# Performance work log

Measured on AMD Instinct MI355X. Metric: run time of the kernel, lower is better.

## Reference

```python
import jax, jax.numpy as jnp
import numpy as np


def setup_inputs() -> dict:
    key = jax.random.key(0)
    ks = jax.random.split(key, 8)
    n_videos, emb_dim = 200000, 128
    n_nodes, k_neigh = 20000, 32
    sc = 1.0 / np.sqrt(emb_dim)
    return {
        "video_embeddings": jax.random.normal(ks[0], (n_videos, emb_dim), jnp.float32),
        "video_nodes": jax.random.randint(ks[1], (n_nodes,), 0, n_videos, jnp.int64 if jax.config.jax_enable_x64 else jnp.int32),
        "neigh_idx": jax.random.randint(ks[2], (n_nodes, k_neigh), 0, n_videos, jnp.int64 if jax.config.jax_enable_x64 else jnp.int32),
        "W1": jax.random.normal(ks[3], (2 * emb_dim, emb_dim), jnp.float32) * sc,
        "b1": jnp.zeros((emb_dim,), jnp.float32),
        "W2": jax.random.normal(ks[4], (emb_dim, emb_dim), jnp.float32) * sc,
        "b2": jnp.zeros((emb_dim,), jnp.float32),
        "W3": jax.random.normal(ks[5], (emb_dim, 1), jnp.float32) * sc,
        "b3": jnp.zeros((1,), jnp.float32),
    }


def reference(video_embeddings, video_nodes, neigh_idx, W1, b1, W2, b2, W3, b3):
    # Ragged per-node loop vectorized as a padded [N, K] neighbor gather.
    neigh_emb = video_embeddings[neigh_idx]          # [N, K, D]
    node_emb = video_embeddings[video_nodes]         # [N, D]
    n, k, d = neigh_emb.shape
    # Attention MLP: cat(neigh, node_repeated) -> relu -> relu -> scalar score
    x = jnp.concatenate([neigh_emb, jnp.broadcast_to(node_emb[:, None, :], (n, k, d))], axis=-1)  # [N, K, 2D]
    h = jax.nn.relu(jnp.einsum("nke,ed->nkd", x, W1) + b1)
    h = jax.nn.relu(jnp.einsum("nke,ed->nkd", h, W2) + b2)
    scores = (jnp.einsum("nkd,do->nko", h, W3) + b3)[..., 0]  # [N, K]
    att = jax.nn.softmax(scores, axis=-1)                      # softmax over neighbors
    # Weighted aggregation: embed_matrix[i] = neigh_emb[i].T @ att[i]
    return jnp.einsum("nkd,nk->nd", neigh_emb, att)
```

## Files before the change

kernel.cpp:

```cpp
#include <hip/hip_runtime.h>
#include <hip/hip_bf16.h>

#define D  128
#define KN 32

typedef __attribute__((ext_vector_type(8))) short bf16x8;
typedef __attribute__((ext_vector_type(4))) float f32x4;

static __device__ __forceinline__ unsigned short f2bf(float f) {
    union { float f; unsigned int u; } v; v.f = f;
    unsigned int u = v.u;
    u += 0x7fff + ((u >> 16) & 1);
    return (unsigned short)(u >> 16);
}
static __device__ __forceinline__ float bf2f(unsigned short h) {
    union { float f; unsigned int u; } v; v.u = ((unsigned int)h) << 16;
    return v.f;
}

__global__ __launch_bounds__(256) void wt_kernel(
    const float* __restrict__ W1, const float* __restrict__ W2,
    unsigned short* __restrict__ W1Tt, unsigned short* __restrict__ W1Tb,
    unsigned short* __restrict__ W2T)
{
    int idx = blockIdx.x * 256 + threadIdx.x;
    if (idx < D * D) {
        int col = idx >> 7, e = idx & 127;
        W1Tt[col * D + e] = f2bf(W1[e * D + col]);
        W1Tb[col * D + e] = f2bf(W1[(D + e) * D + col]);
        W2T [col * D + e] = f2bf(W2[e * D + col]);
    }
}

__global__ __launch_bounds__(256) void p1q_kernel(
    const float* __restrict__ emb, const int* __restrict__ vnodes,
    int NV, int NN, int nvBlocks,
    const unsigned short* __restrict__ W1Tt, const unsigned short* __restrict__ W1Tb,
    const float* __restrict__ b1,
    unsigned short* __restrict__ P1, unsigned short* __restrict__ Q,
    unsigned short* __restrict__ EB)
{
    __shared__ unsigned short sA[128][136];

    const int tid  = threadIdx.x;
    const int lane = tid & 63;
    const int w    = tid >> 6;
    const int m    = lane & 15, q = lane >> 4;

    const bool nv = (int)blockIdx.x < nvBlocks;
    const int  bi = nv ? blockIdx.x : blockIdx.x - nvBlocks;
    const int  M  = nv ? NV : NN;
    const unsigned short* WT = nv ? W1Tt : W1Tb;
    const int r0 = bi * 128;

    int maxRows = M - r0; if (maxRows > 128) maxRows = 128;
    const int maxB = maxRows << 8;

#pragma unroll
    for (int i = 0; i < 16; ++i) {
        int e = tid + 256 * i;
        int row = e >> 5, c4 = (e & 31) << 2;
        int r = r0 + row; if (r > M - 1) r = M - 1;
        int vr = nv ? r : vnodes[r];
        const float4 f = *(const float4*)(emb + (long)vr * D + c4);
        ushort4 h;
        h.x = f2bf(f.x); h.y = f2bf(f.y); h.z = f2bf(f.z); h.w = f2bf(f.w);
        *(ushort4*)(&sA[row][c4]) = h;
    }
    __syncthreads();

    if (nv) {
        char* ebBase = (char*)(EB + (long)r0 * D);
#pragma unroll
        for (int j = 0; j < 8; ++j) {
            int p = j * 4096 + tid * 16;
            if (p < maxB) {
                int row = p >> 8, off = (p & 255) >> 1;
                *(bf16x8*)(ebBase + p) = *(const bf16x8*)(&sA[row][off]);
            }
        }
    }

    bf16x8 Bf[2][4];
#pragma unroll
    for (int nt = 0; nt < 2; ++nt)
#pragma unroll
        for (int kk = 0; kk < 4; ++kk)
            Bf[nt][kk] = *(const bf16x8*)(WT + (32 * w + 16 * nt + m) * D + kk * 32 + q * 8);
    float bv[2];
#pragma unroll
    for (int nt = 0; nt < 2; ++nt) bv[nt] = nv ? 0.f : b1[32 * w + 16 * nt + m];

    f32x4 acc[8][2];
#pragma unroll
    for (int mt = 0; mt < 8; ++mt)
#pragma unroll
        for (int nt = 0; nt < 2; ++nt) acc[mt][nt] = (f32x4){0.f, 0.f, 0.f, 0.f};

#pragma unroll
    for (int kk = 0; kk < 4; ++kk) {
#pragma unroll
        for (int mt = 0; mt < 8; ++mt) {
            bf16x8 a = *(const bf16x8*)(&sA[16 * mt + m][kk * 32 + q * 8]);
            acc[mt][0] = __builtin_amdgcn_mfma_f32_16x16x32_bf16(a, Bf[0][kk], acc[mt][0], 0, 0, 0);
            acc[mt][1] = __builtin_amdgcn_mfma_f32_16x16x32_bf16(a, Bf[1][kk], acc[mt][1], 0, 0, 0);
        }
    }

    __syncthreads();
#pragma unroll
    for (int mt = 0; mt < 8; ++mt)
#pragma unroll
        for (int nt = 0; nt < 2; ++nt) {
            int col = 32 * w + 16 * nt + m;
#pragma unroll
            for (int r = 0; r < 4; ++r)
                sA[16 * mt + 4 * q + r][col] = f2bf(acc[mt][nt][r] + bv[nt]);
        }
    __syncthreads();
    {
        char* dstBase = (char*)((nv ? P1 : Q) + (long)r0 * D);
#pragma unroll
        for (int j = 0; j < 8; ++j) {
            int p = j * 4096 + tid * 16;
            if (p < maxB) {
                int row = p >> 8, off = (p & 255) >> 1;
                *(bf16x8*)(dstBase + p) = *(const bf16x8*)(&sA[row][off]);
            }
        }
    }
}

__global__ __launch_bounds__(256, 3) void agg_kernel(
    const unsigned short* __restrict__ EB, const int* __restrict__ nidx,
    const unsigned short* __restrict__ W2T, const float* __restrict__ b2,
    const float* __restrict__ W3, const float* __restrict__ b3,
    const unsigned short* __restrict__ P1, const unsigned short* __restrict__ Q,
    float* __restrict__ out, int NN)
{
    __shared__ unsigned short sX[128][136];
    __shared__ float sSp[4][128];
    __shared__ float sAtt[128];

    const int tid  = threadIdx.x;
    const int lane = tid & 63;
    const int w    = tid >> 6;
    const int m    = lane & 15, q = lane >> 4;
    const int g4   = q;
    const int c    = m;

    bf16x8 Bf[2][4];
#pragma unroll
    for (int nt = 0; nt < 2; ++nt)
#pragma unroll
        for (int kk = 0; kk < 4; ++kk)
            Bf[nt][kk] = *(const bf16x8*)(W2T + (32 * w + 16 * nt + m) * D + kk * 32 + q * 8);
    float b2v[2], w3v[2];
#pragma unroll
    for (int nt = 0; nt < 2; ++nt) {
        int col = 32 * w + 16 * nt + m;
        b2v[nt] = b2[col];
        w3v[nt] = W3[col];
    }
    const float b3s = b3[0];

    const int groups = (NN + 3) >> 2;

    int g = blockIdx.x;
    int ni[8];
    bf16x8 pf[8];
    if (g < groups) {
        int nd = g * 4 + w; if (nd > NN - 1) nd = NN - 1;
#pragma unroll
        for (int j = 0; j < 8; ++j) {
            ni[j] = nidx[nd * KN + 4 * j + g4];
            pf[j] = *(const bf16x8*)(P1 + (long)ni[j] * D + c * 8);
        }
    }

    for (; g < groups; g += gridDim.x) {
        const int node0 = g * 4;
        int nd = node0 + w; if (nd > NN - 1) nd = NN - 1;

        {
            const bf16x8 qv = *(const bf16x8*)(Q + (long)nd * D + c * 8);
#pragma unroll
            for (int j = 0; j < 8; ++j) {
                bf16x8 r;
#pragma unroll
                for (int h = 0; h < 8; ++h) {
                    float v = bf2f((unsigned short)pf[j][h]) + bf2f((unsigned short)qv[h]);
                    r[h] = (short)f2bf(v > 0.f ? v : 0.f);
                }
                *(bf16x8*)(&sX[w * 32 + 4 * j + g4][c * 8]) = r;
            }
        }

        const int gn = g + gridDim.x;
        const bool more = gn < groups;
        int nin[8];
        if (more) {
            int ndn = gn * 4 + w; if (ndn > NN - 1) ndn = NN - 1;
#pragma unroll
            for (int j = 0; j < 8; ++j) nin[j] = nidx[ndn * KN + 4 * j + g4];
        }

        if (more) {
#pragma unroll
            for (int j = 0; j < 8; ++j)
                pf[j] = *(const bf16x8*)(P1 + (long)nin[j] * D + c * 8);
        }
        __syncthreads();

#pragma unroll
        for (int hv = 0; hv < 2; ++hv) {
            f32x4 acc[4][2];
#pragma unroll
            for (int mt = 0; mt < 4; ++mt) {
                acc[mt][0] = (f32x4){0.f, 0.f, 0.f, 0.f};
                acc[mt][1] = (f32x4){0.f, 0.f, 0.f, 0.f};
            }
#pragma unroll
            for (int kk = 0; kk < 4; ++kk) {
#pragma unroll
                for (int mt = 0; mt < 4; ++mt) {
                    bf16x8 a = *(const bf16x8*)(&sX[16 * (4 * hv + mt) + m][kk * 32 + q * 8]);
                    acc[mt][0] = __builtin_amdgcn_mfma_f32_16x16x32_bf16(a, Bf[0][kk], acc[mt][0], 0, 0, 0);
                    acc[mt][1] = __builtin_amdgcn_mfma_f32_16x16x32_bf16(a, Bf[1][kk], acc[mt][1], 0, 0, 0);
                }
            }
#pragma unroll
            for (int mt = 0; mt < 4; ++mt) {
                float p[4];
#pragma unroll
                for (int r = 0; r < 4; ++r) {
                    float h0 = acc[mt][0][r] + b2v[0]; h0 = h0 > 0.f ? h0 : 0.f;
                    float h1 = acc[mt][1][r] + b2v[1]; h1 = h1 > 0.f ? h1 : 0.f;
                    p[r] = h0 * w3v[0] + h1 * w3v[1];
                }
#pragma unroll
                for (int off = 8; off >= 1; off >>= 1)
#pragma unroll
                    for (int r = 0; r < 4; ++r) p[r] += __shfl_xor(p[r], off, 16);
                if (m == 0) {
#pragma unroll
                    for (int r = 0; r < 4; ++r) sSp[w][16 * (4 * hv + mt) + 4 * q + r] = p[r];
                }
            }
        }

        bf16x8 gv[8];
#pragma unroll
        for (int j = 0; j < 8; ++j)
            gv[j] = *(const bf16x8*)(EB + (long)ni[j] * D + c * 8);
        __syncthreads();

        if (tid < 128) {
            float s = sSp[0][tid] + sSp[1][tid] + sSp[2][tid] + sSp[3][tid] + b3s;
            float mx = s;
#pragma unroll
            for (int off = 16; off >= 1; off >>= 1) mx = fmaxf(mx, __shfl_xor(mx, off, 32));
            float e = __expf(s - mx);
            float sum = e;
#pragma unroll
            for (int off = 16; off >= 1; off >>= 1) sum += __shfl_xor(sum, off, 32);
            sAtt[tid] = e / sum;
        }
        __syncthreads();

        {
            float r8[8] = {0.f, 0.f, 0.f, 0.f, 0.f, 0.f, 0.f, 0.f};
#pragma unroll
            for (int j = 0; j < 8; ++j) {
                float a = sAtt[w * KN + 4 * j + g4];
#pragma unroll
                for (int h = 0; h < 8; ++h)
                    r8[h] += a * bf2f((unsigned short)gv[j][h]);
            }
#pragma unroll
            for (int h = 0; h < 8; ++h) {
                r8[h] += __shfl_xor(r8[h], 16);
                r8[h] += __shfl_xor(r8[h], 32);
            }
            int ndw = node0 + w;
            if (g4 == 0 && ndw < NN) {
                float4 o0 = {r8[0], r8[1], r8[2], r8[3]};
                float4 o1 = {r8[4], r8[5], r8[6], r8[7]};
                *(float4*)(out + (long)ndw * D + c * 8)     = o0;
                *(float4*)(out + (long)ndw * D + c * 8 + 4) = o1;
            }
        }
#pragma unroll
        for (int j = 0; j < 8; ++j) ni[j] = nin[j];
    }
}

__global__ __launch_bounds__(128) void naive_kernel(
    const float* __restrict__ emb, const int* __restrict__ vnodes,
    const int* __restrict__ nidx,
    const float* __restrict__ W1, const float* __restrict__ b1,
    const float* __restrict__ W2, const float* __restrict__ b2,
    const float* __restrict__ W3, const float* __restrict__ b3,
    float* __restrict__ out)
{
    __shared__ float sE[KN + 1][D];
    __shared__ float sH[KN][D];
    __shared__ float sH2[KN][D];
    __shared__ float sS[KN];
    __shared__ float sA2[KN];
    const int node = blockIdx.x, tid = threadIdx.x;

    for (int r = 0; r < KN + 1; ++r) {
        int vr = (r < KN) ? nidx[node * KN + r] : vnodes[node];
        sE[r][tid] = emb[(long)vr * D + tid];
    }
    __syncthreads();
    for (int k = 0; k < KN; ++k) {
        float s = b1[tid];
        for (int e = 0; e < D; ++e) s += sE[k][e]  * W1[e * D + tid];
        for (int e = 0; e < D; ++e) s += sE[KN][e] * W1[(D + e) * D + tid];
        sH[k][tid] = s > 0.f ? s : 0.f;
    }
    __syncthreads();
    for (int k = 0; k < KN; ++k) {
        float s = b2[tid];
        for (int e = 0; e < D; ++e) s += sH[k][e] * W2[e * D + tid];
        sH2[k][tid] = s > 0.f ? s : 0.f;
    }
    __syncthreads();
    if (tid < KN) {
        float s = b3[0];
        for (int e = 0; e < D; ++e) s += sH2[tid][e] * W3[e];
        sS[tid] = s;
    }
    __syncthreads();
    if (tid == 0) {
        float mx = sS[0];
        for (int k = 1; k < KN; ++k) mx = fmaxf(mx, sS[k]);
        float sum = 0.f;
        for (int k = 0; k < KN; ++k) { sA2[k] = __expf(sS[k] - mx); sum += sA2[k]; }
        for (int k = 0; k < KN; ++k) sA2[k] /= sum;
    }
    __syncthreads();
    float a = 0.f;
    for (int k = 0; k < KN; ++k) a += sA2[k] * sE[k][tid];
    out[(long)node * D + tid] = a;
}

extern "C" void kernel_launch(void* const* d_in, const int* in_sizes, int n_in,
                              void* d_out, int out_size, void* d_ws, size_t ws_size,
                              hipStream_t stream) {
    const float* emb    = (const float*)d_in[0];
    const int*   vnodes = (const int*)d_in[1];
    const int*   nidx   = (const int*)d_in[2];
    const float* W1     = (const float*)d_in[3];
    const float* b1     = (const float*)d_in[4];
    const float* W2     = (const float*)d_in[5];
    const float* b2     = (const float*)d_in[6];
    const float* W3     = (const float*)d_in[7];
    const float* b3     = (const float*)d_in[8];
    float* out = (float*)d_out;

    const int NV = in_sizes[0] / D;
    const int NN = in_sizes[1];

    const size_t p1_elems = (size_t)NV * D;
    const size_t q_elems  = (size_t)NN * D;
    const size_t wt_elems = (size_t)D * D;
    const size_t need = (2 * p1_elems + q_elems + 3 * wt_elems) * sizeof(unsigned short);

    if (ws_size >= need) {
        unsigned short* P1   = (unsigned short*)d_ws;
        unsigned short* Q    = P1 + p1_elems;
        unsigned short* W1Tt = Q + q_elems;
        unsigned short* W1Tb = W1Tt + wt_elems;
        unsigned short* W2T  = W1Tb + wt_elems;
        unsigned short* EB   = W2T + wt_elems;

        const int nvBlocks = (NV + 127) / 128;
        const int qBlocks  = (NN + 127) / 128;

        wt_kernel<<<(D * D + 255) / 256, 256, 0, stream>>>(W1, W2, W1Tt, W1Tb, W2T);
        p1q_kernel<<<nvBlocks + qBlocks, 256, 0, stream>>>(
            emb, vnodes, NV, NN, nvBlocks, W1Tt, W1Tb, b1, P1, Q, EB);
        agg_kernel<<<768, 256, 0, stream>>>(
            EB, nidx, W2T, b2, W3, b3, P1, Q, out, NN);
    } else {
        naive_kernel<<<NN, D, 0, stream>>>(emb, vnodes, nidx, W1, b1, W2, b2, W3, b3, out);
    }
}
```

Baseline: 273.8 us.

## Split attention scoring and weighted gather into separate kernels

```diff
diff --git a/kernel.cpp b/kernel.cpp
--- a/kernel.cpp
+++ b/kernel.cpp
@@ -131,16 +131,15 @@
     }
 }
 
-__global__ __launch_bounds__(256, 3) void agg_kernel(
-    const unsigned short* __restrict__ EB, const int* __restrict__ nidx,
+__global__ __launch_bounds__(256, 3) void att_kernel(
+    const int* __restrict__ nidx,
     const unsigned short* __restrict__ W2T, const float* __restrict__ b2,
     const float* __restrict__ W3, const float* __restrict__ b3,
     const unsigned short* __restrict__ P1, const unsigned short* __restrict__ Q,
-    float* __restrict__ out, int NN)
+    float* __restrict__ att, int NN)
 {
     __shared__ unsigned short sX[128][136];
     __shared__ float sSp[4][128];
-    __shared__ float sAtt[128];
 
     const int tid  = threadIdx.x;
     const int lane = tid & 63;
@@ -167,14 +166,13 @@
     const int groups = (NN + 3) >> 2;
 
     int g = blockIdx.x;
-    int ni[8];
     bf16x8 pf[8];
     if (g < groups) {
         int nd = g * 4 + w; if (nd > NN - 1) nd = NN - 1;
 #pragma unroll
         for (int j = 0; j < 8; ++j) {
-            ni[j] = nidx[nd * KN + 4 * j + g4];
-            pf[j] = *(const bf16x8*)(P1 + (long)ni[j] * D + c * 8);
+            int ni = nidx[nd * KN + 4 * j + g4];
+            pf[j] = *(const bf16x8*)(P1 + (long)ni * D + c * 8);
         }
     }
 
@@ -197,18 +195,13 @@
         }
 
         const int gn = g + gridDim.x;
-        const bool more = gn < groups;
-        int nin[8];
-        if (more) {
+        if (gn < groups) {
             int ndn = gn * 4 + w; if (ndn > NN - 1) ndn = NN - 1;
 #pragma unroll
-            for (int j = 0; j < 8; ++j) nin[j] = nidx[ndn * KN + 4 * j + g4];
-        }
-
-        if (more) {
-#pragma unroll
-            for (int j = 0; j < 8; ++j)
-                pf[j] = *(const bf16x8*)(P1 + (long)nin[j] * D + c * 8);
+            for (int j = 0; j < 8; ++j) {
+                int ni = nidx[ndn * KN + 4 * j + g4];
+                pf[j] = *(const bf16x8*)(P1 + (long)ni * D + c * 8);
+            }
         }
         __syncthreads();
 
@@ -248,11 +241,6 @@
                 }
             }
         }
-
-        bf16x8 gv[8];
-#pragma unroll
-        for (int j = 0; j < 8; ++j)
-            gv[j] = *(const bf16x8*)(EB + (long)ni[j] * D + c * 8);
         __syncthreads();
 
         if (tid < 128) {
@@ -264,34 +252,50 @@
             float sum = e;
 #pragma unroll
             for (int off = 16; off >= 1; off >>= 1) sum += __shfl_xor(sum, off, 32);
-            sAtt[tid] = e / sum;
-        }
-        __syncthreads();
-
-        {
-            float r8[8] = {0.f, 0.f, 0.f, 0.f, 0.f, 0.f, 0.f, 0.f};
-#pragma unroll
-            for (int j = 0; j < 8; ++j) {
-                float a = sAtt[w * KN + 4 * j + g4];
-#pragma unroll
-                for (int h = 0; h < 8; ++h)
-                    r8[h] += a * bf2f((unsigned short)gv[j][h]);
-            }
-#pragma unroll
-            for (int h = 0; h < 8; ++h) {
-                r8[h] += __shfl_xor(r8[h], 16);
-                r8[h] += __shfl_xor(r8[h], 32);
-            }
-            int ndw = node0 + w;
-            if (g4 == 0 && ndw < NN) {
-                float4 o0 = {r8[0], r8[1], r8[2], r8[3]};
-                float4 o1 = {r8[4], r8[5], r8[6], r8[7]};
-                *(float4*)(out + (long)ndw * D + c * 8)     = o0;
-                *(float4*)(out + (long)ndw * D + c * 8 + 4) = o1;
-            }
-        }
-#pragma unroll
-        for (int j = 0; j < 8; ++j) ni[j] = nin[j];
+            int an = node0 + (tid >> 5);
+            if (an < NN) att[(long)an * KN + (tid & 31)] = e / sum;
+        }
+    }
+}
+
+__global__ __launch_bounds__(256, 5) void gather_kernel(
+    const unsigned short* __restrict__ EB, const int* __restrict__ nidx,
+    const float* __restrict__ att,
+    float* __restrict__ out, int NN)
+{
+    const int tid  = threadIdx.x;
+    const int lane = tid & 63;
+    const int w    = tid >> 6;
+    const int g4   = lane >> 4, c = lane & 15;
+
+    for (int node = (blockIdx.x << 2) + w; node < NN; node += (gridDim.x << 2)) {
+        float  av[8];
+        bf16x8 gv[8];
+#pragma unroll
+        for (int j = 0; j < 8; ++j) {
+            int k  = 4 * j + g4;
+            int ik = nidx[node * KN + k];
+            av[j]  = att[(long)node * KN + k];
+            gv[j]  = *(const bf16x8*)(EB + (long)ik * D + c * 8);
+        }
+        float r8[8] = {0.f, 0.f, 0.f, 0.f, 0.f, 0.f, 0.f, 0.f};
+#pragma unroll
+        for (int j = 0; j < 8; ++j) {
+            float a = av[j];
+#pragma unroll
+            for (int h = 0; h < 8; ++h) r8[h] += a * bf2f((unsigned short)gv[j][h]);
+        }
+#pragma unroll
+        for (int h = 0; h < 8; ++h) {
+            r8[h] += __shfl_xor(r8[h], 16);
+            r8[h] += __shfl_xor(r8[h], 32);
+        }
+        if (g4 == 0) {
+            float4 o0 = {r8[0], r8[1], r8[2], r8[3]};
+            float4 o1 = {r8[4], r8[5], r8[6], r8[7]};
+            *(float4*)(out + (long)node * D + c * 8)     = o0;
+            *(float4*)(out + (long)node * D + c * 8 + 4) = o1;
+        }
     }
 }
 
@@ -367,7 +371,9 @@
     const size_t p1_elems = (size_t)NV * D;
     const size_t q_elems  = (size_t)NN * D;
     const size_t wt_elems = (size_t)D * D;
-    const size_t need = (2 * p1_elems + q_elems + 3 * wt_elems) * sizeof(unsigned short);
+    const size_t us_elems = 2 * p1_elems + q_elems + 3 * wt_elems;
+    const size_t need = us_elems * sizeof(unsigned short)
+                      + (size_t)NN * KN * sizeof(float);
 
     if (ws_size >= need) {
         unsigned short* P1   = (unsigned short*)d_ws;
@@ -376,6 +382,7 @@
         unsigned short* W1Tb = W1Tt + wt_elems;
         unsigned short* W2T  = W1Tb + wt_elems;
         unsigned short* EB   = W2T + wt_elems;
+        float*          att  = (float*)(EB + p1_elems);
 
         const int nvBlocks = (NV + 127) / 128;
         const int qBlocks  = (NN + 127) / 128;
@@ -383,8 +390,10 @@
         wt_kernel<<<(D * D + 255) / 256, 256, 0, stream>>>(W1, W2, W1Tt, W1Tb, W2T);
         p1q_kernel<<<nvBlocks + qBlocks, 256, 0, stream>>>(
             emb, vnodes, NV, NN, nvBlocks, W1Tt, W1Tb, b1, P1, Q, EB);
-        agg_kernel<<<768, 256, 0, stream>>>(
-            EB, nidx, W2T, b2, W3, b3, P1, Q, out, NN);
+        att_kernel<<<768, 256, 0, stream>>>(
+            nidx, W2T, b2, W3, b3, P1, Q, att, NN);
+        gather_kernel<<<1280, 256, 0, stream>>>(
+            EB, nidx, att, out, NN);
     } else {
         naive_kernel<<<NN, D, 0, stream>>>(emb, vnodes, nidx, W1, b1, W2, b2, W3, b3, out);
     }
```

Result: slower. 283.5 us (+3.5%).
